# Kernel tuning notes

Measured on AMD Instinct MI355X. Metric: run time of the kernel, lower is better.

## Reference

```python
import jax, jax.numpy as jnp
import numpy as np
from jax import lax

B, S, T = 32, 100, 4
NUM_C2, NUM_C3, NUM_D, DV = 500, 2000, 1000, 128


def setup_inputs():
    key = jax.random.key(0)
    ks = jax.random.split(key, 25)
    s = 0.05
    def nrm(k, shape):
        return jax.random.normal(k, shape, dtype=jnp.float32) * s
    return {
        "c2_seq": jax.random.randint(ks[0], (B, S), 0, NUM_C2),
        "c3_seq": jax.random.randint(ks[1], (B, S, T), 1, NUM_C3 + 1),  # 0 is padding; use all-valid tags
        "d_seq": jax.random.randint(ks[2], (B, S), 0, NUM_D),
        "r_seq": jax.random.randint(ks[3], (B, S), 0, 2),
        "D_emb": nrm(ks[4], (NUM_D, 1)),
        "R_emb": nrm(ks[5], (2, DV)),
        "v_c2": nrm(ks[6], (DV,)),
        "v_c3": nrm(ks[7], (DV,)),
        "v_d": nrm(ks[8], (DV,)),
        "W_ih": nrm(ks[9], (3 * DV, 2 * DV)),
        "W_hh": nrm(ks[10], (3 * DV, DV)),
        "b_ih": nrm(ks[11], (3 * DV,)),
        "b_hh": nrm(ks[12], (3 * DV,)),
        "l1_W1": nrm(ks[13], (DV, DV)), "l1_b1": nrm(ks[14], (DV,)),
        "l1_W2": nrm(ks[15], (1, DV)), "l1_b2": nrm(ks[16], (1,)),
        "l2_W1": nrm(ks[17], (DV, 4 * DV)), "l2_b1": nrm(ks[18], (DV,)),
        "l2_W2": nrm(ks[19], (1, DV)), "l2_b2": nrm(ks[20], (1,)),
        "l3_W1": nrm(ks[21], (DV, 4 * DV)), "l3_b1": nrm(ks[22], (DV,)),
        "l3_W2": nrm(ks[23], (1, DV)), "l3_b2": nrm(ks[24], (1,)),
    }


def _mlp(x, W1, b1, W2, b2):
    # Linear -> ReLU -> (Dropout: identity in eval) -> Linear -> (Dropout)
    return jnp.maximum(x @ W1.T + b1, 0.0) @ W2.T + b2


def _gru(x_seq, h0, W_ih, W_hh, b_ih, b_hh):
    # torch.nn.GRU math, batch_first
    def step(h, x):
        gi = x @ W_ih.T + b_ih
        gh = h @ W_hh.T + b_hh
        i_r, i_z, i_n = jnp.split(gi, 3, axis=-1)
        h_r, h_z, h_n = jnp.split(gh, 3, axis=-1)
        r = jax.nn.sigmoid(i_r + h_r)
        z = jax.nn.sigmoid(i_z + h_z)
        n = jnp.tanh(i_n + r * h_n)
        h_new = (1.0 - z) * n + z * h
        return h_new, h_new
    _, hs = lax.scan(step, h0, jnp.swapaxes(x_seq, 0, 1))
    return jnp.swapaxes(hs, 0, 1)


def _forward(c2_seq, c3_seq, d_seq, r_seq, p):
    (D_emb, R_emb, v_c2, v_c3, v_d, W_ih, W_hh, b_ih, b_hh,
     l1_W1, l1_b1, l1_W2, l1_b2, l2_W1, l2_b1, l2_W2, l2_b2,
     l3_W1, l3_b1, l3_W2, l3_b2) = p
    Bn = c2_seq.shape[0]
    gamma = D_emb[d_seq]                      # [B,S,1]
    v_d_seq = gamma * v_d                     # [B,S,DV]
    v_r_seq = R_emb[r_seq]                    # [B,S,DV]
    h0 = jnp.zeros((Bn, DV), dtype=v_d_seq.dtype)
    h_seq = _gru(jnp.concatenate([v_d_seq, v_r_seq], -1), h0, W_ih, W_hh, b_ih, b_hh)
    alpha_seq = _mlp(h_seq, l1_W1, l1_b1, l1_W2, l1_b2)[..., 0]   # [B,S]

    def step(carry, xs):
        C2, C3 = carry
        c2, c3, vd, vr = xs                                      # [B],[B,T],[B,DV],[B,DV]
        mask = (c3 != 0).astype(C3.dtype)                        # [B,T]
        w = mask / mask.sum(-1, keepdims=True)
        beta2 = jnp.take_along_axis(C2, c2[:, None], axis=-1)    # [B,1]
        beta3 = jnp.take_along_axis(C3, c3, axis=-1)             # [B,T]
        beta3_bar = (beta3 * w).sum(-1)                          # [B]
        vc2 = beta2 * v_c2                                       # [B,DV]
        vc3 = beta3[..., None] * v_c3                            # [B,T,DV]
        vc3_bar = beta3_bar[:, None] * v_c3                      # [B,DV]
        new_c2 = _mlp(jnp.concatenate([vc2, vc3_bar, vd, vr], -1),
                      l2_W1, l2_b1, l2_W2, l2_b2)[:, 0]          # [B]
        feat3 = jnp.concatenate([
            jnp.broadcast_to(vc2[:, None, :], vc3.shape), vc3,
            jnp.broadcast_to(vd[:, None, :], vc3.shape),
            jnp.broadcast_to(vr[:, None, :], vc3.shape)], -1)    # [B,T,4*DV]
        new_c3 = _mlp(feat3, l3_W1, l3_b1, l3_W2, l3_b2)[..., 0]  # [B,T]
        oh2 = jax.nn.one_hot(c2, NUM_C2, dtype=C2.dtype)          # [B,NC2]
        oh3 = jax.nn.one_hot(c3, NUM_C3 + 1, dtype=C3.dtype) * mask[..., None]  # [B,T,NC3+1]
        multi = oh3.sum(1)
        C2n = C2 * (1.0 - oh2) + new_c2[:, None] * oh2
        C3n = C3 * (1.0 - multi) + (new_c3[..., None] * oh3).sum(1)
        return (C2n, C3n), (C2n, C3n)

    C2_0 = jnp.zeros((Bn, NUM_C2), dtype=jnp.float32)
    C3_0 = jnp.zeros((Bn, NUM_C3 + 1), dtype=jnp.float32)
    xs = (jnp.swapaxes(c2_seq, 0, 1), jnp.swapaxes(c3_seq, 0, 1),
          jnp.swapaxes(v_d_seq, 0, 1), jnp.swapaxes(v_r_seq, 0, 1))
    _, (C2_seq, C3_seq) = lax.scan(step, (C2_0, C3_0), xs)
    C2_seq = jnp.swapaxes(C2_seq, 0, 1)   # [B,S,NUM_C2]
    C3_seq = jnp.swapaxes(C3_seq, 0, 1)   # [B,S,NUM_C3+1]
    return alpha_seq, h_seq, C2_seq, C3_seq


def reference(c2_seq, c3_seq, d_seq, r_seq, D_emb, R_emb, v_c2, v_c3, v_d,
              W_ih, W_hh, b_ih, b_hh, l1_W1, l1_b1, l1_W2, l1_b2,
              l2_W1, l2_b1, l2_W2, l2_b2, l3_W1, l3_b1, l3_W2, l3_b2):
    p = (D_emb, R_emb, v_c2, v_c3, v_d, W_ih, W_hh, b_ih, b_hh,
         l1_W1, l1_b1, l1_W2, l1_b2, l2_W1, l2_b1, l2_W2, l2_b2,
         l3_W1, l3_b1, l3_W2, l3_b2)
    return _forward(c2_seq, c3_seq, d_seq, r_seq, p)
```

## Files before the change

kernel.cpp:

```cpp
#include <hip/hip_runtime.h>

#define BB   32
#define SS   100
#define TT   4
#define NCC2 500
#define NC3P 2001
#define DD   128

#define HALL 3456
#define LDSF 16256

__device__ __forceinline__ float fast_rcp(float x) { return __builtin_amdgcn_rcpf(x); }
__device__ __forceinline__ float fast_sig(float x) { return fast_rcp(1.f + __expf(-x)); }
__device__ __forceinline__ float fast_tanh(float x) { return 1.f - 2.f * fast_rcp(__expf(2.f * x) + 1.f); }

__device__ __forceinline__ float dpp_sum64(float x) {
    x += __int_as_float(__builtin_amdgcn_update_dpp(0, __float_as_int(x), 0x111, 0xf, 0xf, true));
    x += __int_as_float(__builtin_amdgcn_update_dpp(0, __float_as_int(x), 0x112, 0xf, 0xf, true));
    x += __int_as_float(__builtin_amdgcn_update_dpp(0, __float_as_int(x), 0x114, 0xf, 0xf, true));
    x += __int_as_float(__builtin_amdgcn_update_dpp(0, __float_as_int(x), 0x118, 0xf, 0xf, true));
    x += __int_as_float(__builtin_amdgcn_update_dpp(0, __float_as_int(x), 0x142, 0xa, 0xf, true));
    x += __int_as_float(__builtin_amdgcn_update_dpp(0, __float_as_int(x), 0x143, 0xc, 0xf, true));
    return x;
}

__device__ __forceinline__ float dpp_sum16(float x) {
    x += __int_as_float(__builtin_amdgcn_update_dpp(0, __float_as_int(x), 0x111, 0xf, 0xf, true));
    x += __int_as_float(__builtin_amdgcn_update_dpp(0, __float_as_int(x), 0x112, 0xf, 0xf, true));
    x += __int_as_float(__builtin_amdgcn_update_dpp(0, __float_as_int(x), 0x114, 0xf, 0xf, true));
    x += __int_as_float(__builtin_amdgcn_update_dpp(0, __float_as_int(x), 0x118, 0xf, 0xf, true));
    return x;
}

__device__ __forceinline__ float dot4(float4 a, float4 b) {
    return fmaf(a.x, b.x, fmaf(a.y, b.y, fmaf(a.z, b.z, a.w * b.w)));
}

#define FMA4(W, H) do { a0 = fmaf((W).x, (H).x, a0); a1 = fmaf((W).y, (H).y, a1); \
                        a2 = fmaf((W).z, (H).z, a2); a3 = fmaf((W).w, (H).w, a3); } while (0)

__global__ __launch_bounds__(64) void k_pre(const float* __restrict__ l2W1,
                                            const float* __restrict__ l3W1,
                                            const float* __restrict__ v_c2,
                                            const float* __restrict__ v_c3,
                                            const float* __restrict__ v_d,
                                            const float* __restrict__ Remb,
                                            float* __restrict__ ws)
{
    const int t = threadIdx.x;
    const int g = t >> 4;
    const int c = (t & 15) * 8;
    const float* vsrc = (g == 0) ? v_c2 : (g == 1) ? v_c3 : (g == 2) ? v_d : Remb;
    const float4 va  = *(const float4*)(vsrc + c);
    const float4 vb  = *(const float4*)(vsrc + c + 4);
    const float4 va1 = *(const float4*)(Remb + 128 + c);
    const float4 vb1 = *(const float4*)(Remb + 132 + c);
#pragma unroll
    for (int r = 0; r < 8; ++r) {
        const int row_id = blockIdx.x * 8 + r;
        const float* W = (row_id < 128) ? l2W1 : l3W1;
        float* U = ws + ((row_id < 128) ? 0 : 640);
        const int i = row_id & 127;
        const float* wr = W + i * 512 + g * 128 + c;
        const float4 w0 = *(const float4*)(wr);
        const float4 w1 = *(const float4*)(wr + 4);
        float p  = dot4(w0, va)  + dot4(w1, vb);
        float p1 = dot4(w0, va1) + dot4(w1, vb1);
        p  = dpp_sum16(p);
        p1 = dpp_sum16(p1);
        if ((t & 15) == 15) {
            U[g * 128 + i] = p;
            if (g == 3) U[512 + i] = p1;
        }
    }
}

__global__ __launch_bounds__(768, 1) void k_main(
    const int* __restrict__ c2_seq, const int* __restrict__ c3_seq,
    const int* __restrict__ d_seq,  const int* __restrict__ r_seq,
    const float* __restrict__ D_emb, const float* __restrict__ Remb,
    const float* __restrict__ v_d,
    const float* __restrict__ W_ih, const float* __restrict__ W_hh,
    const float* __restrict__ b_ih, const float* __restrict__ b_hh,
    const float* __restrict__ l2b1, const float* __restrict__ l2W2, const float* __restrict__ l2b2,
    const float* __restrict__ l3b1, const float* __restrict__ l3W2, const float* __restrict__ l3b2,
    const float* __restrict__ ws, float* __restrict__ h_out,
    float* __restrict__ C2o, float* __restrict__ C3o)
{
    __shared__ __align__(16) float sh[LDSF];
    int* shi = (int*)sh;
    const int blk = blockIdx.x;
    const int t = threadIdx.x;

    if (blk < BB) {
        const int b = blk;
        const int p = (t >= 384) ? 1 : 0;
        const int j = t - p * 384;
        const float4* wrow = reinterpret_cast<const float4*>(W_hh + j * DD + p * 64);
        const float4 w0 = wrow[0],  w1 = wrow[1],  w2 = wrow[2],  w3 = wrow[3];
        const float4 w4 = wrow[4],  w5 = wrow[5],  w6 = wrow[6],  w7 = wrow[7];
        const float4 w8 = wrow[8],  w9 = wrow[9],  w10 = wrow[10], w11 = wrow[11];
        const float4 w12 = wrow[12], w13 = wrow[13], w14 = wrow[14], w15 = wrow[15];

        float pd = 0.f, pr0 = 0.f, pr1 = 0.f;
        {
            const float4* wd4 = (const float4*)(W_ih + j * 256 + p * 64);
            const float4* wr4 = (const float4*)(W_ih + j * 256 + 128 + p * 64);
            const float4* vd4 = (const float4*)(v_d + p * 64);
            const float4* r04 = (const float4*)(Remb + p * 64);
            const float4* r14 = (const float4*)(Remb + 128 + p * 64);
#pragma unroll
            for (int k4 = 0; k4 < 16; ++k4) {
                const float4 wd = wd4[k4], wr = wr4[k4];
                const float4 vd = vd4[k4], r0 = r04[k4], r1 = r14[k4];
                pd  = fmaf(wd.x, vd.x, fmaf(wd.y, vd.y, fmaf(wd.z, vd.z, fmaf(wd.w, vd.w, pd))));
                pr0 = fmaf(wr.x, r0.x, fmaf(wr.y, r0.y, fmaf(wr.z, r0.z, fmaf(wr.w, r0.w, pr0))));
                pr1 = fmaf(wr.x, r1.x, fmaf(wr.y, r1.y, fmaf(wr.z, r1.z, fmaf(wr.w, r1.w, pr1))));
            }
        }
        sh[896 + t] = pd; sh[1664 + t] = pr0; sh[2432 + t] = pr1;
        if (t < DD) sh[t] = 0.f;
        if (t < SS) {
            sh[3200 + t]  = D_emb[d_seq[b * SS + t]];
            shi[3300 + t] = r_seq[b * SS + t];
        }
        __syncthreads();

        float gd_r=0,gd_z=0,gd_n=0, g0_r=0,g0_z=0,g0_n=0, g1_r=0,g1_z=0,g1_n=0;
        float bi_r=0,bi_z=0,bi_n=0, bh_r=0,bh_z=0,bh_n=0, h = 0.f;
        if (t < DD) {
            gd_r = sh[896+t]      + sh[896+t+384];
            gd_z = sh[896+t+128]  + sh[896+t+512];
            gd_n = sh[896+t+256]  + sh[896+t+640];
            g0_r = sh[1664+t]     + sh[1664+t+384];
            g0_z = sh[1664+t+128] + sh[1664+t+512];
            g0_n = sh[1664+t+256] + sh[1664+t+640];
            g1_r = sh[2432+t]     + sh[2432+t+384];
            g1_z = sh[2432+t+128] + sh[2432+t+512];
            g1_n = sh[2432+t+256] + sh[2432+t+640];
            bi_r = b_ih[t]; bi_z = b_ih[t+128]; bi_n = b_ih[t+256];
            bh_r = b_hh[t]; bh_z = b_hh[t+128]; bh_n = b_hh[t+256];
        }
        __syncthreads();

        for (int s = 0; s < SS; ++s) {
            float a0 = 0.f, a1 = 0.f, a2 = 0.f, a3 = 0.f;
            const float4* hv4 = reinterpret_cast<const float4*>(sh) + p * 16;
            float4 h0 = hv4[0], h1 = hv4[1], h2 = hv4[2], h3 = hv4[3];
            FMA4(w0, h0); FMA4(w1, h1); FMA4(w2, h2); FMA4(w3, h3);
            h0 = hv4[4]; h1 = hv4[5]; h2 = hv4[6]; h3 = hv4[7];
            FMA4(w4, h0); FMA4(w5, h1); FMA4(w6, h2); FMA4(w7, h3);
            h0 = hv4[8]; h1 = hv4[9]; h2 = hv4[10]; h3 = hv4[11];
            FMA4(w8, h0); FMA4(w9, h1); FMA4(w10, h2); FMA4(w11, h3);
            h0 = hv4[12]; h1 = hv4[13]; h2 = hv4[14]; h3 = hv4[15];
            FMA4(w12, h0); FMA4(w13, h1); FMA4(w14, h2); FMA4(w15, h3);
            sh[128 + t] = (a0 + a1) + (a2 + a3);
            __syncthreads();
            if (t < DD) {
                float ghr = sh[128+t]     + sh[128+t+384] + bh_r;
                float ghz = sh[128+t+128] + sh[128+t+512] + bh_z;
                float ghn = sh[128+t+256] + sh[128+t+640] + bh_n;
                float gamma = sh[3200 + s]; int rr = shi[3300 + s];
                float gir = fmaf(gamma, gd_r, (rr ? g1_r : g0_r) + bi_r);
                float giz = fmaf(gamma, gd_z, (rr ? g1_z : g0_z) + bi_z);
                float gin = fmaf(gamma, gd_n, (rr ? g1_n : g0_n) + bi_n);
                float r = fast_sig(gir + ghr);
                float z = fast_sig(giz + ghz);
                float n = fast_tanh(fmaf(r, ghn, gin));
                h = (1.f - z) * n + z * h;
                sh[t] = h;
                sh[HALL + s * DD + t] = h;
            }
            __syncthreads();
        }

        {
            const float4* hsrc = reinterpret_cast<const float4*>(sh + HALL);
            float4* hdst = reinterpret_cast<float4*>(h_out + (size_t)b * SS * DD);
            for (int i = t; i < SS * DD / 4; i += 768) hdst[i] = hsrc[i];
        }
    } else if (t < 64) {
        const int b = blk - BB;
        float* C2s = sh;
        float* C3s = sh + NCC2;
        for (int k = t; k < NCC2 + NC3P; k += 64) sh[k] = 0.f;
        for (int k = t; k < SS; k += 64) {
            shi[2501 + k] = c2_seq[b * SS + k];
            sh[3004 + k]  = D_emb[d_seq[b * SS + k]];
            shi[3104 + k] = r_seq[b * SS + k];
        }
        for (int k = t; k < SS; k += 64)
            reinterpret_cast<int4*>(shi + 2604)[k] = reinterpret_cast<const int4*>(c3_seq + b * SS * TT)[k];

        const float* u2 = ws;
        const float* u3 = ws + 640;
        const float u2a0 = u2[t],        u2a1 = u2[64 + t];
        const float u2b0 = u2[128 + t],  u2b1 = u2[192 + t];
        const float u2c0 = u2[256 + t],  u2c1 = u2[320 + t];
        const float u2d00 = u2[384 + t], u2d01 = u2[448 + t];
        const float u2d10 = u2[512 + t], u2d11 = u2[576 + t];
        const float u3a0 = u3[t],        u3a1 = u3[64 + t];
        const float u3b0 = u3[128 + t],  u3b1 = u3[192 + t];
        const float u3c0 = u3[256 + t],  u3c1 = u3[320 + t];
        const float u3d00 = u3[384 + t], u3d01 = u3[448 + t];
        const float u3d10 = u3[512 + t], u3d11 = u3[576 + t];
        const float b2_0 = l2b1[t], b2_1 = l2b1[64 + t];
        const float w2_0 = l2W2[t], w2_1 = l2W2[64 + t];
        const float b3_0 = l3b1[t], b3_1 = l3b1[64 + t];
        const float w3_0 = l3W2[t], w3_1 = l3W2[64 + t];
        const float c2bias = l2b2[0], c3bias = l3b2[0];

        int  nc2 = shi[2501];
        int4 nc3 = reinterpret_cast<const int4*>(shi + 2604)[0];
        float ngam = sh[3004];
        int   nrr  = shi[3104];

        for (int s = 0; s < SS; ++s) {
            const int rs = b * SS + s;
            const int c2i = nc2;
            const int i0 = nc3.x, i1 = nc3.y, i2 = nc3.z, i3 = nc3.w;
            const float gamma = ngam;
            const int rr = nrr;
            if (s + 1 < SS) {
                nc2 = shi[2501 + s + 1];
                nc3 = reinterpret_cast<const int4*>(shi + 2604)[s + 1];
                ngam = sh[3004 + s + 1];
                nrr  = shi[3104 + s + 1];
            }

            const float beta2 = C2s[c2i];
            const bool k0 = (i0 != 0), k1 = (i1 != 0), k2 = (i2 != 0), k3 = (i3 != 0);
            const float m0 = k0 ? 1.f : 0.f, m1 = k1 ? 1.f : 0.f;
            const float m2 = k2 ? 1.f : 0.f, m3 = k3 ? 1.f : 0.f;
            const float bt0 = C3s[i0], bt1 = C3s[i1], bt2 = C3s[i2], bt3 = C3s[i3];
            const float msum = m0 + m1 + m2 + m3;
            const float b3bar = (bt0 * m0 + bt1 * m1 + bt2 * m2 + bt3 * m3) * fast_rcp(msum);

            const float ud20 = rr ? u2d10 : u2d00, ud21 = rr ? u2d11 : u2d01;
            const float ud30 = rr ? u3d10 : u3d00, ud31 = rr ? u3d11 : u3d01;

            float h20 = fmaf(beta2, u2a0, fmaf(b3bar, u2b0, fmaf(gamma, u2c0, ud20 + b2_0)));
            float h21 = fmaf(beta2, u2a1, fmaf(b3bar, u2b1, fmaf(gamma, u2c1, ud21 + b2_1)));
            float newc2 = dpp_sum64(fmaf(fmaxf(h20, 0.f), w2_0, fmaxf(h21, 0.f) * w2_1)) + c2bias;

            const float base30 = fmaf(beta2, u3a0, fmaf(gamma, u3c0, ud30 + b3_0));
            const float base31 = fmaf(beta2, u3a1, fmaf(gamma, u3c1, ud31 + b3_1));
            float ha, hb, q0, q1, q2, q3;
            ha = fmaf(bt0, u3b0, base30); hb = fmaf(bt0, u3b1, base31);
            q0 = dpp_sum64(fmaf(fmaxf(ha, 0.f), w3_0, fmaxf(hb, 0.f) * w3_1)) + c3bias;
            ha = fmaf(bt1, u3b0, base30); hb = fmaf(bt1, u3b1, base31);
            q1 = dpp_sum64(fmaf(fmaxf(ha, 0.f), w3_0, fmaxf(hb, 0.f) * w3_1)) + c3bias;
            ha = fmaf(bt2, u3b0, base30); hb = fmaf(bt2, u3b1, base31);
            q2 = dpp_sum64(fmaf(fmaxf(ha, 0.f), w3_0, fmaxf(hb, 0.f) * w3_1)) + c3bias;
            ha = fmaf(bt3, u3b0, base30); hb = fmaf(bt3, u3b1, base31);
            q3 = dpp_sum64(fmaf(fmaxf(ha, 0.f), w3_0, fmaxf(hb, 0.f) * w3_1)) + c3bias;

            float val0, val1, val2, val3;
            {
                float c = m0 + ((k1 && i1 == i0) ? 1.f : 0.f) + ((k2 && i2 == i0) ? 1.f : 0.f) + ((k3 && i3 == i0) ? 1.f : 0.f);
                float qs = (k0 ? q0 : 0.f) + ((k1 && i1 == i0) ? q1 : 0.f) + ((k2 && i2 == i0) ? q2 : 0.f) + ((k3 && i3 == i0) ? q3 : 0.f);
                val0 = bt0 * (1.f - c) + qs;
            }
            {
                float c = ((k0 && i0 == i1) ? 1.f : 0.f) + m1 + ((k2 && i2 == i1) ? 1.f : 0.f) + ((k3 && i3 == i1) ? 1.f : 0.f);
                float qs = ((k0 && i0 == i1) ? q0 : 0.f) + (k1 ? q1 : 0.f) + ((k2 && i2 == i1) ? q2 : 0.f) + ((k3 && i3 == i1) ? q3 : 0.f);
                val1 = bt1 * (1.f - c) + qs;
            }
            {
                float c = ((k0 && i0 == i2) ? 1.f : 0.f) + ((k1 && i1 == i2) ? 1.f : 0.f) + m2 + ((k3 && i3 == i2) ? 1.f : 0.f);
                float qs = ((k0 && i0 == i2) ? q0 : 0.f) + ((k1 && i1 == i2) ? q1 : 0.f) + (k2 ? q2 : 0.f) + ((k3 && i3 == i2) ? q3 : 0.f);
                val2 = bt2 * (1.f - c) + qs;
            }
            {
                float c = ((k0 && i0 == i3) ? 1.f : 0.f) + ((k1 && i1 == i3) ? 1.f : 0.f) + ((k2 && i2 == i3) ? 1.f : 0.f) + m3;
                float qs = ((k0 && i0 == i3) ? q0 : 0.f) + ((k1 && i1 == i3) ? q1 : 0.f) + ((k2 && i2 == i3) ? q2 : 0.f) + (k3 ? q3 : 0.f);
                val3 = bt3 * (1.f - c) + qs;
            }

            if (t == 63) {
                C2s[c2i] = newc2;
                if (k0) C3s[i0] = val0;
                if (k1) C3s[i1] = val1;
                if (k2) C3s[i2] = val2;
                if (k3) C3s[i3] = val3;
            }

            float* c2row = C2o + (size_t)rs * NCC2;
            float* c3row = C3o + (size_t)rs * NC3P;
            *reinterpret_cast<float4*>(c2row + 4 * t) = *reinterpret_cast<const float4*>(C2s + 4 * t);
            if (t < 61)
                *reinterpret_cast<float4*>(c2row + 256 + 4 * t) = *reinterpret_cast<const float4*>(C2s + 256 + 4 * t);
            const int p0 = (4 - (rs & 3)) & 3;
            if (p0 == 0) {
#pragma unroll
                for (int i = 0; i < 8; ++i) {
                    int d4 = i * 64 + t;
                    if (d4 < 500)
                        reinterpret_cast<float4*>(c3row)[d4] = reinterpret_cast<const float4*>(C3s)[d4];
                }
                if (t == 0) c3row[2000] = C3s[2000];
            } else {
                const int tail = (2001 - p0) & 3;
                const int dt = 2001 - tail;
                if (t < p0) c3row[t] = C3s[t];
                if (t < tail) c3row[dt + t] = C3s[dt + t];
#pragma unroll
                for (int i = 0; i < 8; ++i) {
                    int d = p0 + 4 * (i * 64 + t);
                    if (d + 3 <= 2000) {
                        float4 v;
                        v.x = C3s[d]; v.y = C3s[d + 1]; v.z = C3s[d + 2]; v.w = C3s[d + 3];
                        *reinterpret_cast<float4*>(c3row + d) = v;
                    }
                }
            }
        }
    }
}

__global__ __launch_bounds__(256) void k_alpha2(const float* __restrict__ h_seq,
                                                const float* __restrict__ W1,
                                                const float* __restrict__ b1,
                                                const float* __restrict__ W2,
                                                const float* __restrict__ b2,
                                                float* __restrict__ alpha)
{
    __shared__ float part[256];
    __shared__ float red[2];
    const int t = threadIdx.x;
    const int ch = t & 127, half = t >> 7;
    const float4* w4 = (const float4*)(W1 + ch * 128 + half * 64);
    float4 w[16];
#pragma unroll
    for (int i = 0; i < 16; ++i) w[i] = w4[i];
    const float b1v = b1[ch];
    const float w2v = W2[ch];
    const float b2v = b2[0];
    const int base = blockIdx.x * 16;
    for (int r = 0; r < 16; ++r) {
        const float* h = h_seq + (size_t)(base + r) * 128 + half * 64;
        float a0 = 0.f, a1 = 0.f, a2 = 0.f, a3 = 0.f;
#pragma unroll
        for (int i = 0; i < 16; ++i) {
            float4 hv = *(const float4*)(h + 4 * i);
            a0 = fmaf(w[i].x, hv.x, a0); a1 = fmaf(w[i].y, hv.y, a1);
            a2 = fmaf(w[i].z, hv.z, a2); a3 = fmaf(w[i].w, hv.w, a3);
        }
        part[t] = (a0 + a1) + (a2 + a3);
        __syncthreads();
        if (t < 128) {
            float v = fmaxf(part[t] + part[t + 128] + b1v, 0.f) * w2v;
            v = dpp_sum64(v);
            if ((t & 63) == 63) red[t >> 6] = v;
        }
        __syncthreads();
        if (t == 0) alpha[base + r] = red[0] + red[1] + b2v;
    }
}

extern "C" void kernel_launch(void* const* d_in, const int* in_sizes, int n_in,
                              void* d_out, int out_size, void* d_ws, size_t ws_size,
                              hipStream_t stream)
{
    (void)in_sizes; (void)n_in; (void)out_size; (void)ws_size;
    const int*   c2_seq = (const int*)d_in[0];
    const int*   c3_seq = (const int*)d_in[1];
    const int*   d_seq  = (const int*)d_in[2];
    const int*   r_seq  = (const int*)d_in[3];
    const float* D_emb  = (const float*)d_in[4];
    const float* Remb   = (const float*)d_in[5];
    const float* v_c2   = (const float*)d_in[6];
    const float* v_c3   = (const float*)d_in[7];
    const float* v_d    = (const float*)d_in[8];
    const float* W_ih   = (const float*)d_in[9];
    const float* W_hh   = (const float*)d_in[10];
    const float* b_ih   = (const float*)d_in[11];
    const float* b_hh   = (const float*)d_in[12];
    const float* l1W1   = (const float*)d_in[13];
    const float* l1b1   = (const float*)d_in[14];
    const float* l1W2   = (const float*)d_in[15];
    const float* l1b2   = (const float*)d_in[16];
    const float* l2W1   = (const float*)d_in[17];
    const float* l2b1   = (const float*)d_in[18];
    const float* l2W2   = (const float*)d_in[19];
    const float* l2b2   = (const float*)d_in[20];
    const float* l3W1   = (const float*)d_in[21];
    const float* l3b1   = (const float*)d_in[22];
    const float* l3W2   = (const float*)d_in[23];
    const float* l3b2   = (const float*)d_in[24];

    float* out   = (float*)d_out;
    float* alpha = out;
    float* h_out = out + 3200;
    float* C2o   = out + 412800;
    float* C3o   = out + 2012800;
    float* ws    = (float*)d_ws;

    k_pre<<<32, 64, 0, stream>>>(l2W1, l3W1, v_c2, v_c3, v_d, Remb, ws);
    k_main<<<2 * BB, 768, 0, stream>>>(c2_seq, c3_seq, d_seq, r_seq, D_emb, Remb, v_d,
                                       W_ih, W_hh, b_ih, b_hh,
                                       l2b1, l2W2, l2b2, l3b1, l3W2, l3b2,
                                       ws, h_out, C2o, C3o);
    k_alpha2<<<200, 256, 0, stream>>>(h_out, l1W1, l1b1, l1W2, l1b2, alpha);
}
```

Baseline: 129.0 us.

## Fuse alpha MLP into GRU blocks and pin W_hh registers with asm barriers

Removes the separate k_alpha2 launch and computes the l1 MLP (alpha) inside each GRU block after the recurrence, reading the h sequence directly from LDS instead of re-reading it from global memory. Each group of 256 threads processes one timestep row, so three rows are handled per iteration. It also converts the W_hh register weights to ext_vector floats and adds empty asm barriers to keep them resident in VGPRs. The trade-off is that one kernel launch and a global round trip are removed, but the alpha work now runs serially on only 32 blocks instead of 200 and adds register pressure.

```diff
diff --git a/kernel.cpp b/kernel.cpp
--- a/kernel.cpp
+++ b/kernel.cpp
@@ -9,6 +9,8 @@
 
 #define HALL 3456
 #define LDSF 16256
+
+typedef float f4 __attribute__((ext_vector_type(4)));
 
 __device__ __forceinline__ float fast_rcp(float x) { return __builtin_amdgcn_rcpf(x); }
 __device__ __forceinline__ float fast_sig(float x) { return fast_rcp(1.f + __expf(-x)); }
@@ -82,9 +84,11 @@
     const float* __restrict__ v_d,
     const float* __restrict__ W_ih, const float* __restrict__ W_hh,
     const float* __restrict__ b_ih, const float* __restrict__ b_hh,
+    const float* __restrict__ l1W1, const float* __restrict__ l1b1,
+    const float* __restrict__ l1W2, const float* __restrict__ l1b2,
     const float* __restrict__ l2b1, const float* __restrict__ l2W2, const float* __restrict__ l2b2,
     const float* __restrict__ l3b1, const float* __restrict__ l3W2, const float* __restrict__ l3b2,
-    const float* __restrict__ ws, float* __restrict__ h_out,
+    const float* __restrict__ ws, float* __restrict__ alpha, float* __restrict__ h_out,
     float* __restrict__ C2o, float* __restrict__ C3o)
 {
     __shared__ __align__(16) float sh[LDSF];
@@ -96,11 +100,15 @@
         const int b = blk;
         const int p = (t >= 384) ? 1 : 0;
         const int j = t - p * 384;
-        const float4* wrow = reinterpret_cast<const float4*>(W_hh + j * DD + p * 64);
-        const float4 w0 = wrow[0],  w1 = wrow[1],  w2 = wrow[2],  w3 = wrow[3];
-        const float4 w4 = wrow[4],  w5 = wrow[5],  w6 = wrow[6],  w7 = wrow[7];
-        const float4 w8 = wrow[8],  w9 = wrow[9],  w10 = wrow[10], w11 = wrow[11];
-        const float4 w12 = wrow[12], w13 = wrow[13], w14 = wrow[14], w15 = wrow[15];
+        const f4* wrow = reinterpret_cast<const f4*>(W_hh + j * DD + p * 64);
+        f4 w0 = wrow[0],  w1 = wrow[1],  w2 = wrow[2],  w3 = wrow[3];
+        f4 w4 = wrow[4],  w5 = wrow[5],  w6 = wrow[6],  w7 = wrow[7];
+        f4 w8 = wrow[8],  w9 = wrow[9],  w10 = wrow[10], w11 = wrow[11];
+        f4 w12 = wrow[12], w13 = wrow[13], w14 = wrow[14], w15 = wrow[15];
+        asm volatile("" : "+v"(w0), "+v"(w1), "+v"(w2), "+v"(w3),
+                          "+v"(w4), "+v"(w5), "+v"(w6), "+v"(w7));
+        asm volatile("" : "+v"(w8), "+v"(w9), "+v"(w10), "+v"(w11),
+                          "+v"(w12), "+v"(w13), "+v"(w14), "+v"(w15));
 
         float pd = 0.f, pr0 = 0.f, pr1 = 0.f;
         {
@@ -145,8 +153,8 @@
 
         for (int s = 0; s < SS; ++s) {
             float a0 = 0.f, a1 = 0.f, a2 = 0.f, a3 = 0.f;
-            const float4* hv4 = reinterpret_cast<const float4*>(sh) + p * 16;
-            float4 h0 = hv4[0], h1 = hv4[1], h2 = hv4[2], h3 = hv4[3];
+            const f4* hv4 = reinterpret_cast<const f4*>(sh) + p * 16;
+            f4 h0 = hv4[0], h1 = hv4[1], h2 = hv4[2], h3 = hv4[3];
             FMA4(w0, h0); FMA4(w1, h1); FMA4(w2, h2); FMA4(w3, h3);
             h0 = hv4[4]; h1 = hv4[5]; h2 = hv4[6]; h3 = hv4[7];
             FMA4(w4, h0); FMA4(w5, h1); FMA4(w6, h2); FMA4(w7, h3);
@@ -179,6 +187,46 @@
             float4* hdst = reinterpret_cast<float4*>(h_out + (size_t)b * SS * DD);
             for (int i = t; i < SS * DD / 4; i += 768) hdst[i] = hsrc[i];
         }
+
+        {
+            const int g = t >> 8, tt = t & 255;
+            const int ch = tt & 127, half = tt >> 7;
+            const float4* aw4 = (const float4*)(l1W1 + ch * 128 + half * 64);
+            float4 aw[16];
+#pragma unroll
+            for (int i = 0; i < 16; ++i) aw[i] = aw4[i];
+            if (t < 128) { sh[768 + t] = l1b1[t]; sh[896 + t] = l1W2[t]; }
+            __syncthreads();
+            for (int it = 0; it < 34; ++it) {
+                const int r = it * 3 + g;
+                const bool act = (r < SS);
+                float val = 0.f;
+                if (act) {
+                    const float* hrow = sh + HALL + r * 128 + half * 64;
+                    float a0 = 0.f, a1 = 0.f, a2 = 0.f, a3 = 0.f;
+#pragma unroll
+                    for (int i = 0; i < 16; ++i) {
+                        float4 hv = *(const float4*)(hrow + 4 * i);
+                        a0 = fmaf(aw[i].x, hv.x, a0); a1 = fmaf(aw[i].y, hv.y, a1);
+                        a2 = fmaf(aw[i].z, hv.z, a2); a3 = fmaf(aw[i].w, hv.w, a3);
+                    }
+                    val = (a0 + a1) + (a2 + a3);
+                }
+                sh[t] = val;
+                __syncthreads();
+                if (t < 384) {
+                    const int g2 = t >> 7, ch2 = t & 127;
+                    float v = fmaxf(sh[g2 * 256 + ch2] + sh[g2 * 256 + 128 + ch2] + sh[768 + ch2], 0.f) * sh[896 + ch2];
+                    v = dpp_sum64(v);
+                    if ((t & 63) == 63) sh[1024 + (t >> 6)] = v;
+                }
+                __syncthreads();
+                if (t < 3) {
+                    const int r2 = it * 3 + t;
+                    if (r2 < SS) alpha[b * SS + r2] = sh[1024 + 2 * t] + sh[1024 + 2 * t + 1] + l1b2[0];
+                }
+            }
+        }
     } else if (t < 64) {
         const int b = blk - BB;
         float* C2s = sh;
@@ -315,46 +363,6 @@
                 }
             }
         }
-    }
-}
-
-__global__ __launch_bounds__(256) void k_alpha2(const float* __restrict__ h_seq,
-                                                const float* __restrict__ W1,
-                                                const float* __restrict__ b1,
-                                                const float* __restrict__ W2,
-                                                const float* __restrict__ b2,
-                                                float* __restrict__ alpha)
-{
-    __shared__ float part[256];
-    __shared__ float red[2];
-    const int t = threadIdx.x;
-    const int ch = t & 127, half = t >> 7;
-    const float4* w4 = (const float4*)(W1 + ch * 128 + half * 64);
-    float4 w[16];
-#pragma unroll
-    for (int i = 0; i < 16; ++i) w[i] = w4[i];
-    const float b1v = b1[ch];
-    const float w2v = W2[ch];
-    const float b2v = b2[0];
-    const int base = blockIdx.x * 16;
-    for (int r = 0; r < 16; ++r) {
-        const float* h = h_seq + (size_t)(base + r) * 128 + half * 64;
-        float a0 = 0.f, a1 = 0.f, a2 = 0.f, a3 = 0.f;
-#pragma unroll
-        for (int i = 0; i < 16; ++i) {
-            float4 hv = *(const float4*)(h + 4 * i);
-            a0 = fmaf(w[i].x, hv.x, a0); a1 = fmaf(w[i].y, hv.y, a1);
-            a2 = fmaf(w[i].z, hv.z, a2); a3 = fmaf(w[i].w, hv.w, a3);
-        }
-        part[t] = (a0 + a1) + (a2 + a3);
-        __syncthreads();
-        if (t < 128) {
-            float v = fmaxf(part[t] + part[t + 128] + b1v, 0.f) * w2v;
-            v = dpp_sum64(v);
-            if ((t & 63) == 63) red[t >> 6] = v;
-        }
-        __syncthreads();
-        if (t == 0) alpha[base + r] = red[0] + red[1] + b2v;
     }
 }
 
@@ -399,7 +407,7 @@
     k_pre<<<32, 64, 0, stream>>>(l2W1, l3W1, v_c2, v_c3, v_d, Remb, ws);
     k_main<<<2 * BB, 768, 0, stream>>>(c2_seq, c3_seq, d_seq, r_seq, D_emb, Remb, v_d,
                                        W_ih, W_hh, b_ih, b_hh,
+                                       l1W1, l1b1, l1W2, l1b2,
                                        l2b1, l2W2, l2b2, l3b1, l3W2, l3b2,
-                                       ws, h_out, C2o, C3o);
-    k_alpha2<<<200, 256, 0, stream>>>(h_out, l1W1, l1b1, l1W2, l1b2, alpha);
-}
+                                       ws, alpha, h_out, C2o, C3o);
+}
```

After: 142.1 us. +10.2%, slower.
